# Kernel tuning notes

Measured on AMD Instinct MI355X. Metric: run time of the kernel, lower is better.

The kernel has to match this reference:

```python
import jax, jax.numpy as jnp
import numpy as np

N_COMPANY = 16384
N_SECTOR = 64
PER_SECTOR = N_COMPANY // N_SECTOR  # 256, companies grouped contiguously by sector
WIN = 32
D_IN = 16
H_GRU = 64
H_INTRA = 64
H_INTER = 64
D_OUT = 4
E_INNER = 524288  # avg degree 32 within sectors


def setup_inputs() -> dict:
    key = jax.random.key(0)
    ks = jax.random.split(key, 20)
    s = 0.05

    daily_data_batch = jax.random.normal(ks[0], (WIN, N_COMPANY, D_IN), jnp.float32)

    rng = np.random.default_rng(0)
    dst = rng.integers(0, N_COMPANY, E_INNER)
    src = (dst // PER_SECTOR) * PER_SECTOR + rng.integers(0, PER_SECTOR, E_INNER)  # same-sector neighbors
    inner_edge = jnp.asarray(np.stack([src, dst]), jnp.int32)

    a, b = np.meshgrid(np.arange(N_SECTOR), np.arange(N_SECTOR), indexing="ij")
    oe = np.stack([a.ravel(), b.ravel()])
    oe = oe[:, oe[0] != oe[1]]  # fully-connected sector graph w/o self loops (GAT adds them)
    outer_edge = jnp.asarray(oe, jnp.int32)

    sector_ids = jnp.asarray(np.arange(N_COMPANY) // PER_SECTOR, jnp.int32)

    inp = {
        "daily_data_batch": daily_data_batch,
        "inner_edge": inner_edge,
        "outer_edge": outer_edge,
        "sector_ids": sector_ids,
        # BatchNorm1d(input_dim*window_size)
        "bn_gamma": jnp.ones((D_IN * WIN,), jnp.float32),
        "bn_beta": jnp.zeros((D_IN * WIN,), jnp.float32),
        # Graph GRU (per-node learnable initial hidden state)
        "gru_Wih": s * jax.random.normal(ks[1], (D_IN, 3 * H_GRU), jnp.float32),
        "gru_Whh": s * jax.random.normal(ks[2], (H_GRU, 3 * H_GRU), jnp.float32),
        "gru_bih": jnp.zeros((3 * H_GRU,), jnp.float32),
        "gru_bhh": jnp.zeros((3 * H_GRU,), jnp.float32),
        "gru_h0": s * jax.random.normal(ks[3], (N_COMPANY, H_GRU), jnp.float32),
        # intra-sector GATConv
        "gat1_W": s * jax.random.normal(ks[4], (H_GRU, H_INTRA), jnp.float32),
        "gat1_asrc": s * jax.random.normal(ks[5], (H_INTRA,), jnp.float32),
        "gat1_adst": s * jax.random.normal(ks[6], (H_INTRA,), jnp.float32),
        "gat1_b": jnp.zeros((H_INTRA,), jnp.float32),
        # inter-sector GATConv
        "gat2_W": s * jax.random.normal(ks[7], (H_INTRA, H_INTER), jnp.float32),
        "gat2_asrc": s * jax.random.normal(ks[8], (H_INTER,), jnp.float32),
        "gat2_adst": s * jax.random.normal(ks[9], (H_INTER,), jnp.float32),
        "gat2_b": jnp.zeros((H_INTER,), jnp.float32),
        # fusion / logit heads
        "fusion_W": s * jax.random.normal(ks[10], (H_GRU + H_INTRA + H_INTER, H_GRU), jnp.float32),
        "fusion_b": jnp.zeros((H_GRU,), jnp.float32),
        "logit_W": s * jax.random.normal(ks[11], (H_GRU, D_OUT), jnp.float32),
        "logit_b": jnp.zeros((D_OUT,), jnp.float32),
    }
    return inp


def _gat(x, edge, W, a_src, a_dst, b):
    """PyG-style single-head GATConv with default add_self_loops=True."""
    N = x.shape[0]
    h = x @ W  # [N, F]
    loops = jnp.arange(N, dtype=edge.dtype)
    src = jnp.concatenate([edge[0], loops])
    dst = jnp.concatenate([edge[1], loops])
    e = jax.nn.leaky_relu(h[src] @ a_src + h[dst] @ a_dst, 0.2)  # [E]
    # segment softmax over incoming edges per dst node
    m = jax.ops.segment_max(e, dst, num_segments=N)
    ex = jnp.exp(e - m[dst])
    denom = jax.ops.segment_sum(ex, dst, num_segments=N)
    alpha = ex / (denom[dst] + 1e-16)
    out = jax.ops.segment_sum(h[src] * alpha[:, None], dst, num_segments=N)
    return out + b


def _forward(daily_data_batch, inner_edge, outer_edge, sector_ids,
             bn_gamma, bn_beta,
             gru_Wih, gru_Whh, gru_bih, gru_bhh, gru_h0,
             gat1_W, gat1_asrc, gat1_adst, gat1_b,
             gat2_W, gat2_asrc, gat2_adst, gat2_b,
             fusion_W, fusion_b, logit_W, logit_b):
    W, N, D = daily_data_batch.shape
    # BatchNorm1d over companies (train-mode batch stats, eps=1e-5)
    xb = jnp.transpose(daily_data_batch, (1, 0, 2)).reshape(N, W * D)
    mu = xb.mean(axis=0)
    var = xb.var(axis=0)
    xb = (xb - mu) * jax.lax.rsqrt(var + 1e-5) * bn_gamma + bn_beta
    x = jnp.transpose(xb.reshape(N, W, D), (1, 0, 2))  # [W, N, D]

    # GRU over the window, per-node hidden state
    def step(h, xt):
        gi = xt @ gru_Wih + gru_bih
        gh = h @ gru_Whh + gru_bhh
        ir, iz, inn = jnp.split(gi, 3, axis=-1)
        hr, hz, hn = jnp.split(gh, 3, axis=-1)
        r = jax.nn.sigmoid(ir + hr)
        z = jax.nn.sigmoid(iz + hz)
        n = jnp.tanh(inn + r * hn)
        return (1.0 - z) * n + z * h, None

    seq_emb, _ = jax.lax.scan(step, gru_h0, x)  # [N, H_GRU]

    intra_emb = _gat(seq_emb, inner_edge, gat1_W, gat1_asrc, gat1_adst, gat1_b)  # [N, H_INTRA]

    # sector_separater + per-sector max pooling == segment_max
    sec_pool = jax.ops.segment_max(intra_emb, sector_ids, num_segments=N_SECTOR)  # [S, H_INTRA]
    sec_emb = _gat(sec_pool, outer_edge, gat2_W, gat2_asrc, gat2_adst, gat2_b)  # [S, H_INTER]
    sec_broad = sec_emb[sector_ids]  # repeat_interleave back to companies

    fusion_vec = jnp.concatenate([seq_emb, sec_broad, intra_emb], axis=-1)
    fusion_vec = jax.nn.relu(fusion_vec @ fusion_W + fusion_b)
    logits = jax.nn.softmax(fusion_vec @ logit_W + logit_b, axis=1)
    logits = jnp.cumsum(logits, axis=1)
    eps = 5e-08
    return jnp.clip(logits, eps, 1.0 - eps)


def reference(daily_data_batch, inner_edge, outer_edge, sector_ids,
              bn_gamma, bn_beta,
              gru_Wih, gru_Whh, gru_bih, gru_bhh, gru_h0,
              gat1_W, gat1_asrc, gat1_adst, gat1_b,
              gat2_W, gat2_asrc, gat2_adst, gat2_b,
              fusion_W, fusion_b, logit_W, logit_b):
    return _forward(daily_data_batch, inner_edge, outer_edge, sector_ids,
                    bn_gamma, bn_beta,
                    gru_Wih, gru_Whh, gru_bih, gru_bhh, gru_h0,
                    gat1_W, gat1_asrc, gat1_adst, gat1_b,
                    gat2_W, gat2_asrc, gat2_adst, gat2_b,
                    fusion_W, fusion_b, logit_W, logit_b)
```

## Files before the change

### kernel.cpp

```cpp
#include <hip/hip_runtime.h>

#define NC 16384
#define WIN 32
#define DI 16
#define EI 524288

typedef unsigned short u16;
typedef unsigned char u8;
typedef unsigned int u32;
typedef __attribute__((ext_vector_type(8))) short bfrag8;
typedef __attribute__((ext_vector_type(4))) float facc4;

__device__ __forceinline__ float bf2f(u16 u) { return __uint_as_float(((u32)u) << 16); }
__device__ __forceinline__ u16 f2bf(float f) {
    u32 u = __float_as_uint(f);
    u += 0x7FFFu + ((u >> 16) & 1u);
    return (u16)(u >> 16);
}
__device__ __forceinline__ float frcp(float x) { return __builtin_amdgcn_rcpf(x); }
__device__ __forceinline__ float ex2(float x) {
#if __has_builtin(__builtin_amdgcn_exp2f)
    return __builtin_amdgcn_exp2f(x);
#else
    return __expf(x * 0.69314718055994531f);
#endif
}
__device__ __forceinline__ u32 pk2bf(float a, float b) {
    u32 r;
    asm("v_cvt_pk_bf16_f32 %0, %1, %2" : "=v"(r) : "v"(a), "v"(b));
    return r;
}
__device__ __forceinline__ float lrelu(float x) { return x >= 0.0f ? x : 0.2f * x; }
__device__ __forceinline__ float loadf(const void* p, size_t i, bool f32) {
    return f32 ? ((const float*)p)[i] : bf2f(((const u16*)p)[i]);
}
__device__ __forceinline__ bool is_f32(const void* gamma) {
    return ((const u32*)gamma)[0] == 0x3F800000u;
}

#define O_WIMG  1024
#define O_BIMG  10240
#define O_BIH   16384
#define O_BHH   16576
#define O_G1W   16768
#define O_G1AS  20864
#define O_G1AD  20928
#define O_G1B   20992
#define O_G2W   21056
#define O_G2AS  25152
#define O_G2AD  25216
#define O_G2B   25280
#define O_FB    25344
#define O_LW    25408
#define O_LB    25664
#define O_FW16  25668
#define O_BNACC 31812
#define O_SEQ   40960
#define O_H1    1089536
#define O_INTRA 1613824
#define O_SPOOL 2138112
#define O_AS    2170880
#define O_AD    2187264
#define O_M     2203648

__global__ __launch_bounds__(256) void k_convert(const void* __restrict__ gamma,
                                                 const void* __restrict__ wih,
                                                 const void* __restrict__ whh,
                                                 const void* __restrict__ bih,
                                                 const void* __restrict__ bhh,
                                                 const void* __restrict__ g1w,
                                                 const void* __restrict__ g1as,
                                                 const void* __restrict__ g1ad,
                                                 const void* __restrict__ g1b,
                                                 const void* __restrict__ g2w,
                                                 const void* __restrict__ g2as,
                                                 const void* __restrict__ g2ad,
                                                 const void* __restrict__ g2b,
                                                 const void* __restrict__ fw,
                                                 const void* __restrict__ fb,
                                                 const void* __restrict__ lw,
                                                 const void* __restrict__ lb,
                                                 float* __restrict__ ws,
                                                 uint4* __restrict__ M16) {
    int gt = blockIdx.x * 256 + threadIdx.x;
    const int GS = 64 * 256;
    bool f32 = is_f32(gamma);
    const float KR = -1.4426950408889634f;
    const float KN = -2.8853900817779268f;
    u16* fw16 = (u16*)(ws + O_FW16);
    for (int i = gt; i < 12288; i += GS)
        fw16[i] = f32 ? f2bf(((const float*)fw)[i]) : ((const u16*)fw)[i];
    for (int i = gt; i < 4096; i += GS) {
        ws[O_G1W + i] = loadf(g1w, i, f32);
        ws[O_G2W + i] = loadf(g2w, i, f32);
    }
    if (gt < 64) {
        ws[O_G1AS + gt] = loadf(g1as, gt, f32);
        ws[O_G1AD + gt] = loadf(g1ad, gt, f32);
        ws[O_G1B + gt] = loadf(g1b, gt, f32);
        ws[O_G2AS + gt] = loadf(g2as, gt, f32);
        ws[O_G2AD + gt] = loadf(g2ad, gt, f32);
        ws[O_G2B + gt] = loadf(g2b, gt, f32);
        ws[O_FB + gt] = loadf(fb, gt, f32);
    }
    if (gt < 256) ws[O_LW + gt] = loadf(lw, gt, f32);
    if (gt < 4) ws[O_LB + gt] = loadf(lb, gt, f32);
    for (int i = gt; i < 1024; i += GS) ws[O_BNACC + i] = 0.f;
    const uint4 z4 = {0u, 0u, 0u, 0u};
    for (int i = gt; i < 262144; i += GS) M16[i] = z4;

    for (int i = gt; i < 9216; i += GS) {
        int trow = i / 36;
        int idx = i % 36;
        int w_ = trow >> 6, lane_ = trow & 63, li_ = lane_ & 15, q_ = lane_ >> 4;
        u16 lo, hi;
        if (idx < 24) {
            int g = idx >> 3, kc = (idx >> 2) & 1, j2 = idx & 3;
            float sc = (g < 2) ? KR : KN;
            int col = g * 64 + w_ * 16 + li_;
            int k = kc * 32 + q_ * 8 + j2 * 2;
            lo = f2bf(sc * loadf(whh, (size_t)k * 192 + col, f32));
            hi = f2bf(sc * loadf(whh, (size_t)(k + 1) * 192 + col, f32));
        } else {
            int idx2 = idx - 24;
            int g = idx2 >> 2, j2 = idx2 & 3;
            float sc = (g < 2) ? KR : KN;
            int col = g * 64 + w_ * 16 + li_;
            int k = q_ * 8 + j2 * 2;
            lo = (k < 16) ? f2bf(sc * loadf(wih, (size_t)k * 192 + col, f32)) : (u16)0;
            hi = (k + 1 < 16) ? f2bf(sc * loadf(wih, (size_t)(k + 1) * 192 + col, f32)) : (u16)0;
        }
        ((u32*)(ws + O_WIMG))[i] = (u32)lo | ((u32)hi << 16);
    }
    for (int i = gt; i < 1024; i += GS) {
        int trow = i >> 2, e = i & 3;
        int w_ = trow >> 6, lane_ = trow & 63, li_ = lane_ & 15;
        int c = w_ * 16 + li_;
        float v;
        if (e == 0) v = KR * (loadf(bih, c, f32) + loadf(bhh, c, f32));
        else if (e == 1) v = KR * (loadf(bih, 64 + c, f32) + loadf(bhh, 64 + c, f32));
        else if (e == 2) v = KN * loadf(bih, 128 + c, f32);
        else v = KN * loadf(bhh, 128 + c, f32);
        ws[O_BIMG + i] = v;
    }
}

__global__ __launch_bounds__(256) void k_prep(const void* __restrict__ daily,
                                              const void* __restrict__ gamma,
                                              float* __restrict__ bnacc,
                                              const int* __restrict__ edges,
                                              u32* __restrict__ M32) {
    __shared__ float rS[256 * 17];
    __shared__ float rQ[256 * 17];
    int bid = blockIdx.x;
    int tid = threadIdx.x;
    if (bid >= 128) {
        int g = (bid - 128) * 256 + tid;
        int4 s4 = ((const int4*)edges)[g];
        int4 d4 = ((const int4*)(edges + EI))[g];
        int ss[4] = {s4.x, s4.y, s4.z, s4.w};
        int dd[4] = {d4.x, d4.y, d4.z, d4.w};
#pragma unroll
        for (int i = 0; i < 4; i++) {
            int sl = ss[i] & 255;
            atomicAdd(&M32[dd[i] * 64 + (sl >> 2)], 1u << ((sl & 3) * 8));
        }
        return;
    }
    int w = bid >> 2, ch = bid & 3;
    bool f32 = is_f32(gamma);
    float s[16], q[16];
#pragma unroll
    for (int i = 0; i < 16; i++) { s[i] = 0.f; q[i] = 0.f; }
    for (int it = 0; it < 16; it++) {
        int c = ch * 4096 + it * 256 + tid;
        size_t base = ((size_t)w * NC + c) * DI;
        float v[16];
        if (f32) {
            const float4* p = (const float4*)((const float*)daily + base);
            float4 a = p[0], b = p[1], cc = p[2], d = p[3];
            v[0] = a.x; v[1] = a.y; v[2] = a.z; v[3] = a.w;
            v[4] = b.x; v[5] = b.y; v[6] = b.z; v[7] = b.w;
            v[8] = cc.x; v[9] = cc.y; v[10] = cc.z; v[11] = cc.w;
            v[12] = d.x; v[13] = d.y; v[14] = d.z; v[15] = d.w;
        } else {
            const uint4* p = (const uint4*)((const u16*)daily + base);
            uint4 a = p[0], b = p[1];
            u32 us[8] = {a.x, a.y, a.z, a.w, b.x, b.y, b.z, b.w};
#pragma unroll
            for (int i = 0; i < 8; i++) {
                v[2 * i] = __uint_as_float(us[i] << 16);
                v[2 * i + 1] = __uint_as_float(us[i] & 0xFFFF0000u);
            }
        }
#pragma unroll
        for (int i = 0; i < 16; i++) { s[i] += v[i]; q[i] += v[i] * v[i]; }
    }
#pragma unroll
    for (int i = 0; i < 16; i++) { rS[tid * 17 + i] = s[i]; rQ[tid * 17 + i] = q[i]; }
    __syncthreads();
    int f = tid & 15, g = tid >> 4;
    float ss = 0.f, qq = 0.f;
    for (int t = g * 16; t < g * 16 + 16; t++) { ss += rS[t * 17 + f]; qq += rQ[t * 17 + f]; }
    atomicAdd(&bnacc[w * 16 + f], ss);
    atomicAdd(&bnacc[512 + w * 16 + f], qq);
}

__global__ __launch_bounds__(256) void k_gru(const void* __restrict__ daily,
                                             const void* __restrict__ gamma,
                                             const void* __restrict__ beta,
                                             const void* __restrict__ h0_g,
                                             const float* __restrict__ ws,
                                             float* __restrict__ seq_out,
                                             u16* __restrict__ h1_out,
                                             float* __restrict__ asg,
                                             float* __restrict__ adg) {
    __shared__ __attribute__((aligned(16))) u16 sHd[2][16 * 72];
    __shared__ __attribute__((aligned(16))) u16 sXall[512 * 24];
    __shared__ float sSc[512], sSh[512];
    __shared__ float sRed[2][4][16];
    int tid = threadIdx.x;
    int w = tid >> 6, lane = tid & 63;
    int li = lane & 15, q = lane >> 4;
    int n0 = blockIdx.x * 16;
    int colw = w * 16 + li;
    bool f32 = is_f32(gamma);

    for (int f = tid; f < 512; f += 256) {
        float mu = ws[O_BNACC + f] * (1.0f / NC);
        float var = ws[O_BNACC + 512 + f] * (1.0f / NC) - mu * mu;
        float sc = loadf(gamma, f, f32) * rsqrtf(var + 1e-5f);
        sSc[f] = sc;
        sSh[f] = loadf(beta, f, f32) - mu * sc;
    }
    __syncthreads();

    for (int R = tid; R < 512; R += 256) {
        int t = R >> 4, m = R & 15;
        size_t base = ((size_t)t * NC + n0 + m) * DI;
        float xv[16];
        if (f32) {
            const float4* p = (const float4*)((const float*)daily + base);
            float4 a = p[0], b = p[1], c = p[2], d = p[3];
            xv[0] = a.x; xv[1] = a.y; xv[2] = a.z; xv[3] = a.w;
            xv[4] = b.x; xv[5] = b.y; xv[6] = b.z; xv[7] = b.w;
            xv[8] = c.x; xv[9] = c.y; xv[10] = c.z; xv[11] = c.w;
            xv[12] = d.x; xv[13] = d.y; xv[14] = d.z; xv[15] = d.w;
        } else {
            const uint4* p = (const uint4*)((const u16*)daily + base);
            uint4 a = p[0], b = p[1];
            u32 us[8] = {a.x, a.y, a.z, a.w, b.x, b.y, b.z, b.w};
#pragma unroll
            for (int i = 0; i < 8; i++) {
                xv[2 * i] = __uint_as_float(us[i] << 16);
                xv[2 * i + 1] = __uint_as_float(us[i] & 0xFFFF0000u);
            }
        }
        u32 pxu[8];
#pragma unroll
        for (int i = 0; i < 16; i += 2)
            pxu[i >> 1] = pk2bf(xv[i] * sSc[t * 16 + i] + sSh[t * 16 + i],
                                xv[i + 1] * sSc[t * 16 + i + 1] + sSh[t * 16 + i + 1]);
        *(uint4*)&sXall[R * 24] = *(const uint4*)&pxu[0];
        *(uint4*)&sXall[R * 24 + 8] = *(const uint4*)&pxu[4];
    }

    bfrag8 bh[3][2];
    bfrag8 bx[3];
    {
        const bfrag8* wf = (const bfrag8*)((const char*)(ws + O_WIMG) + (size_t)tid * 144);
        int c_ = 0;
#pragma unroll
        for (int g = 0; g < 3; g++)
#pragma unroll
            for (int kc = 0; kc < 2; kc++) bh[g][kc] = wf[c_++];
#pragma unroll
        for (int g = 0; g < 3; g++) bx[g] = wf[c_++];
    }
    float bR, bZ, bNX, bNH;
    {
        float4 b0 = ((const float4*)(ws + O_BIMG))[tid];
        bR = b0.x; bZ = b0.y; bNX = b0.z; bNH = b0.w;
    }

    float hC[4];
#pragma unroll
    for (int r = 0; r < 4; r++)
        hC[r] = loadf(h0_g, (size_t)(n0 + q * 4 + r) * 64 + colw, f32);
    {
        int hr = tid >> 4, hc = (tid & 15) * 4;
        u32 a = pk2bf(loadf(h0_g, (size_t)(n0 + hr) * 64 + hc, f32),
                      loadf(h0_g, (size_t)(n0 + hr) * 64 + hc + 1, f32));
        u32 b = pk2bf(loadf(h0_g, (size_t)(n0 + hr) * 64 + hc + 2, f32),
                      loadf(h0_g, (size_t)(n0 + hr) * 64 + hc + 3, f32));
        uint2 v2; v2.x = a; v2.y = b;
        *(uint2*)&sHd[0][hr * 72 + hc] = v2;
    }
    __syncthreads();

    bfrag8 ax = (bfrag8){0, 0, 0, 0, 0, 0, 0, 0};
    if (q < 2) ax = *(const bfrag8*)&sXall[li * 24 + q * 8];
    for (int t = 0; t < WIN; t++) {
        int p = t & 1;
        bfrag8 ah0 = *(const bfrag8*)&sHd[p][li * 72 + q * 8];
        bfrag8 ah1 = *(const bfrag8*)&sHd[p][li * 72 + 32 + q * 8];
        int tn = (t + 1) & (WIN - 1);
        bfrag8 axn = (bfrag8){0, 0, 0, 0, 0, 0, 0, 0};
        if (q < 2) axn = *(const bfrag8*)&sXall[(tn * 16 + li) * 24 + q * 8];
        facc4 aR = __builtin_amdgcn_mfma_f32_16x16x32_bf16(ax, bx[0], (facc4){bR, bR, bR, bR}, 0, 0, 0);
        facc4 aZ = __builtin_amdgcn_mfma_f32_16x16x32_bf16(ax, bx[1], (facc4){bZ, bZ, bZ, bZ}, 0, 0, 0);
        facc4 aNX = __builtin_amdgcn_mfma_f32_16x16x32_bf16(ax, bx[2], (facc4){bNX, bNX, bNX, bNX}, 0, 0, 0);
        facc4 aNH = __builtin_amdgcn_mfma_f32_16x16x32_bf16(ah0, bh[2][0], (facc4){bNH, bNH, bNH, bNH}, 0, 0, 0);
        aR = __builtin_amdgcn_mfma_f32_16x16x32_bf16(ah0, bh[0][0], aR, 0, 0, 0);
        aZ = __builtin_amdgcn_mfma_f32_16x16x32_bf16(ah0, bh[1][0], aZ, 0, 0, 0);
        aNH = __builtin_amdgcn_mfma_f32_16x16x32_bf16(ah1, bh[2][1], aNH, 0, 0, 0);
        aR = __builtin_amdgcn_mfma_f32_16x16x32_bf16(ah1, bh[0][1], aR, 0, 0, 0);
        aZ = __builtin_amdgcn_mfma_f32_16x16x32_bf16(ah1, bh[1][1], aZ, 0, 0, 0);
#pragma unroll
        for (int r = 0; r < 4; r++) {
            float gr = frcp(1.0f + ex2(aR[r]));
            float gz = frcp(1.0f + ex2(aZ[r]));
            float narg = aNX[r] + gr * aNH[r];
            float gn = 2.0f * frcp(1.0f + ex2(narg)) - 1.0f;
            hC[r] = gn + gz * (hC[r] - gn);
        }
#pragma unroll
        for (int rp = 0; rp < 4; rp += 2) {
            u32 pk = pk2bf(hC[rp], hC[rp + 1]);
            sHd[p ^ 1][(q * 4 + rp) * 72 + colw] = (u16)pk;
            sHd[p ^ 1][(q * 4 + rp + 1) * 72 + colw] = (u16)(pk >> 16);
        }
        __syncthreads();
        ax = axn;
    }

#pragma unroll
    for (int r = 0; r < 4; r++)
        seq_out[(size_t)(n0 + q * 4 + r) * 64 + colw] = hC[r];

    bfrag8 a0 = *(const bfrag8*)&sHd[0][li * 72 + q * 8];
    bfrag8 a1 = *(const bfrag8*)&sHd[0][li * 72 + 32 + q * 8];
    const facc4 zf = {0.f, 0.f, 0.f, 0.f};
    bfrag8 bg0, bg1;
#pragma unroll
    for (int j = 0; j < 8; j++) {
        bg0[j] = (short)f2bf(ws[O_G1W + (q * 8 + j) * 64 + colw]);
        bg1[j] = (short)f2bf(ws[O_G1W + (32 + q * 8 + j) * 64 + colw]);
    }
    facc4 acc = __builtin_amdgcn_mfma_f32_16x16x32_bf16(a0, bg0, zf, 0, 0, 0);
    acc = __builtin_amdgcn_mfma_f32_16x16x32_bf16(a1, bg1, acc, 0, 0, 0);
    float a1s_j = ws[O_G1AS + colw], a1d_j = ws[O_G1AD + colw];
    float pAs[4], pAd[4];
#pragma unroll
    for (int r = 0; r < 4; r++) {
        h1_out[(size_t)(n0 + q * 4 + r) * 64 + colw] = f2bf(acc[r]);
        pAs[r] = acc[r] * a1s_j;
        pAd[r] = acc[r] * a1d_j;
    }
#pragma unroll
    for (int o = 1; o < 16; o <<= 1)
#pragma unroll
        for (int r = 0; r < 4; r++) {
            pAs[r] += __shfl_xor(pAs[r], o);
            pAd[r] += __shfl_xor(pAd[r], o);
        }
    if (li == 0) {
#pragma unroll
        for (int r = 0; r < 4; r++) {
            sRed[0][w][q * 4 + r] = pAs[r];
            sRed[1][w][q * 4 + r] = pAd[r];
        }
    }
    __syncthreads();
    if (tid < 16) {
        asg[n0 + tid] = sRed[0][0][tid] + sRed[0][1][tid] + sRed[0][2][tid] + sRed[0][3][tid];
        adg[n0 + tid] = sRed[1][0][tid] + sRed[1][1][tid] + sRed[1][2][tid] + sRed[1][3][tid];
    }
}

__global__ __launch_bounds__(256) void k_gat1agg(const u16* __restrict__ h1g,
                                                 const float* __restrict__ ws,
                                                 const u8* __restrict__ M8,
                                                 const float* __restrict__ asg,
                                                 const float* __restrict__ adg,
                                                 u16* __restrict__ intra,
                                                 float* __restrict__ spool8) {
    __shared__ __attribute__((aligned(16))) u16 hT[64 * 264];
    __shared__ __attribute__((aligned(16))) u16 sP[32 * 264];
    __shared__ float sAs[256], sAd[32], sB[64], sRS[32];
    __shared__ float sRSp[8][32];
    __shared__ float wmax[4];
    int tid = threadIdx.x;
    int sector = blockIdx.x >> 3;
    int dstbase = sector * 256 + (blockIdx.x & 7) * 32;
    int sbase = sector * 256;
    {
#pragma unroll
        for (int p = 0; p < 8; p++) {
            int row = p * 32 + (tid >> 3);
            int c0 = (tid & 7) * 8;
            uint4 v = *(const uint4*)(h1g + (size_t)(sbase + row) * 64 + c0);
            u16 e[8];
            *(uint4*)e = v;
#pragma unroll
            for (int i = 0; i < 8; i++) hT[(c0 + i) * 264 + row] = e[i];
        }
    }
    sAs[tid] = asg[sbase + tid];
    if (tid < 32) sAd[tid] = adg[dstbase + tid];
    if (tid < 64) sB[tid] = ws[O_G1B + tid];
    __syncthreads();
    int lane = tid & 63, w = tid >> 6;
    int li = lane & 15, q = lane >> 4;
    {
        float a = sAs[tid];
#pragma unroll
        for (int o = 1; o < 64; o <<= 1) a = fmaxf(a, __shfl_xor(a, o));
        if (lane == 0) wmax[w] = a;
    }
    __syncthreads();
    float maxA = fmaxf(fmaxf(wmax[0], wmax[1]), fmaxf(wmax[2], wmax[3]));

    int prow = tid >> 3, pcg = tid & 7;
    {
        float adr_p = sAd[prow];
        float mrow_p = lrelu(maxA + adr_p);
        float lsum = 0.f;
        const u8* mp = M8 + (size_t)(dstbase + prow) * 256 + pcg * 32;
        uint4 mva = *(const uint4*)mp;
        uint4 mvb = *(const uint4*)(mp + 16);
        u32 wsrc[8] = {mva.x, mva.y, mva.z, mva.w, mvb.x, mvb.y, mvb.z, mvb.w};
#pragma unroll
        for (int i2 = 0; i2 < 16; i2++) {
            int i0 = 2 * i2;
            u32 mb0 = (wsrc[i0 >> 2] >> ((i0 & 3) * 8)) & 255u;
            u32 mb1 = (wsrc[i0 >> 2] >> (((i0 + 1) & 3) * 8)) & 255u;
            int c = pcg * 32 + i0;
            float e0 = lrelu(sAs[c] + adr_p);
            float e1 = lrelu(sAs[c + 1] + adr_p);
            float v0 = (float)mb0 * __expf(e0 - mrow_p);
            float v1 = (float)mb1 * __expf(e1 - mrow_p);
            u16 b0 = f2bf(v0), b1 = f2bf(v1);
            *(u32*)&sP[prow * 264 + pcg * 32 + i0] = (u32)b0 | ((u32)b1 << 16);
            lsum += bf2f(b0) + bf2f(b1);
        }
        sRSp[pcg][prow] = lsum;
    }
    __syncthreads();

    facc4 acc[2];
    acc[0] = (facc4){0.f, 0.f, 0.f, 0.f};
    acc[1] = (facc4){0.f, 0.f, 0.f, 0.f};
#pragma unroll
    for (int kc = 0; kc < 8; kc++) {
        bfrag8 bfh = *(const bfrag8*)&hT[(w * 16 + li) * 264 + kc * 32 + q * 8];
#pragma unroll
        for (int mt = 0; mt < 2; mt++) {
            bfrag8 af = *(const bfrag8*)&sP[(mt * 16 + li) * 264 + kc * 32 + q * 8];
            acc[mt] = __builtin_amdgcn_mfma_f32_16x16x32_bf16(af, bfh, acc[mt], 0, 0, 0);
        }
    }
    if (tid < 32) {
        float s = 0.f;
#pragma unroll
        for (int g = 0; g < 8; g++) s += sRSp[g][tid];
        sRS[tid] = s;
    }
    __syncthreads();

    float vmax = -1e30f;
    int colL = w * 16 + li;
#pragma unroll
    for (int mt = 0; mt < 2; mt++) {
#pragma unroll
        for (int r = 0; r < 4; r++) {
            int row = mt * 16 + q * 4 + r;
            int d = dstbase + row;
            int selfI = (blockIdx.x & 7) * 32 + row;
            float adr = sAd[row];
            float es = lrelu(sAs[selfI] + adr);
            float mrow = lrelu(maxA + adr);
            float exS = __expf(es - mrow);
            float denom = sRS[row] + exS;
            float inv = frcp(denom + 1e-16f);
            float selfh = bf2f(hT[colL * 264 + selfI]);
            float val = (acc[mt][r] + exS * selfh) * inv + sB[colL];
            intra[(size_t)d * 64 + colL] = f2bf(val);
            vmax = fmaxf(vmax, val);
        }
    }
    vmax = fmaxf(vmax, __shfl_xor(vmax, 16));
    vmax = fmaxf(vmax, __shfl_xor(vmax, 32));
    if (q == 0) spool8[(size_t)blockIdx.x * 64 + colL] = vmax;
}

__global__ __launch_bounds__(256) void k_fusion(const float* __restrict__ seq,
                                                const float* __restrict__ spool8,
                                                const u16* __restrict__ intra,
                                                const float* __restrict__ ws,
                                                const void* __restrict__ gamma,
                                                void* __restrict__ out) {
    __shared__ __attribute__((aligned(16))) union {
        struct { u16 sPmax[64 * 72]; float sH2[64 * 68]; } p0;
        struct { u16 sV[64 * 200]; float sFus[64 * 68]; } p1;
    } U;
    __shared__ float sSemb[64], sAs2[64], sAd2[64];
    __shared__ float sFB[64], sLW[256], sLB[4];
    __shared__ float red2[512];
    int tid = threadIdx.x, n0 = blockIdx.x * 64;
    int sid = blockIdx.x >> 2;
    bool f32 = is_f32(gamma);
    int lane = tid & 63, w = tid >> 6;
    int li = lane & 15, q = lane >> 4;
    int colw = w * 16 + li;

    for (int i = tid; i < 4096; i += 256) {
        int n = i >> 6, k = i & 63;
        const float* pp = &spool8[(size_t)(n * 8) * 64 + k];
        float m = pp[0];
#pragma unroll
        for (int p = 1; p < 8; p++) m = fmaxf(m, pp[p * 64]);
        U.p0.sPmax[n * 72 + k] = f2bf(m);
    }
    bfrag8 bw2[2];
#pragma unroll
    for (int kc = 0; kc < 2; kc++)
#pragma unroll
        for (int j = 0; j < 8; j++)
            bw2[kc][j] = (short)f2bf(ws[O_G2W + (kc * 32 + q * 8 + j) * 64 + colw]);
    __syncthreads();
    {
        const facc4 zf = {0.f, 0.f, 0.f, 0.f};
#pragma unroll
        for (int mt = 0; mt < 4; mt++) {
            bfrag8 af0 = *(const bfrag8*)&U.p0.sPmax[(mt * 16 + li) * 72 + q * 8];
            bfrag8 af1 = *(const bfrag8*)&U.p0.sPmax[(mt * 16 + li) * 72 + 32 + q * 8];
            facc4 a2 = __builtin_amdgcn_mfma_f32_16x16x32_bf16(af0, bw2[0], zf, 0, 0, 0);
            a2 = __builtin_amdgcn_mfma_f32_16x16x32_bf16(af1, bw2[1], a2, 0, 0, 0);
#pragma unroll
            for (int r = 0; r < 4; r++)
                U.p0.sH2[(mt * 16 + q * 4 + r) * 68 + colw] = a2[r];
        }
    }
    __syncthreads();
    {
        int n = tid >> 2, jg = tid & 3, j0 = jg * 16;
        float ps = 0.f, pd = 0.f;
#pragma unroll
        for (int i = 0; i < 16; i++) {
            float v = U.p0.sH2[n * 68 + j0 + i];
            ps += v * ws[O_G2AS + j0 + i];
            pd += v * ws[O_G2AD + j0 + i];
        }
        red2[(n * 4 + jg) * 2] = ps;
        red2[(n * 4 + jg) * 2 + 1] = pd;
    }
    __syncthreads();
    if (tid < 64) {
        float s = 0.f, dd = 0.f;
        for (int g = 0; g < 4; g++) { s += red2[(tid * 4 + g) * 2]; dd += red2[(tid * 4 + g) * 2 + 1]; }
        sAs2[tid] = s; sAd2[tid] = dd;
    }
    __syncthreads();
    if (tid < 64) {
        float e = lrelu(sAs2[tid] + sAd2[sid]);
        float m = e;
        for (int o = 32; o; o >>= 1) m = fmaxf(m, __shfl_xor(m, o));
        float ex = __expf(e - m);
        float den = ex;
        for (int o = 32; o; o >>= 1) den += __shfl_xor(den, o);
        float inv = frcp(den + 1e-16f);
        float o_ = 0.f;
        for (int l = 0; l < 64; l++) {
            float a = __shfl(ex, l);
            o_ += a * U.p0.sH2[l * 68 + tid];
        }
        sSemb[tid] = o_ * inv + ws[O_G2B + tid];
    }
    if (tid < 64) sFB[tid] = ws[O_FB + tid];
    sLW[tid] = ws[O_LW + tid];
    if (tid < 4) sLB[tid] = ws[O_LB + tid];
    __syncthreads();

    {
        int c = tid >> 2, p = tid & 3;
        u16 px[16];
        const float* rp = seq + (size_t)(n0 + c) * 64 + p * 16;
#pragma unroll
        for (int i = 0; i < 16; i += 4) {
            float4 v = *(const float4*)&rp[i];
            px[i] = f2bf(v.x); px[i + 1] = f2bf(v.y); px[i + 2] = f2bf(v.z); px[i + 3] = f2bf(v.w);
        }
        *(uint4*)&U.p1.sV[c * 200 + p * 16] = *(const uint4*)&px[0];
        *(uint4*)&U.p1.sV[c * 200 + p * 16 + 8] = *(const uint4*)&px[8];
#pragma unroll
        for (int i = 0; i < 16; i++) px[i] = f2bf(sSemb[p * 16 + i]);
        *(uint4*)&U.p1.sV[c * 200 + 64 + p * 16] = *(const uint4*)&px[0];
        *(uint4*)&U.p1.sV[c * 200 + 64 + p * 16 + 8] = *(const uint4*)&px[8];
        const u16* ip = intra + (size_t)(n0 + c) * 64 + p * 16;
        *(uint4*)&U.p1.sV[c * 200 + 128 + p * 16] = *(const uint4*)ip;
        *(uint4*)&U.p1.sV[c * 200 + 128 + p * 16 + 8] = *(const uint4*)(ip + 8);
    }
    const u16* fw16g = (const u16*)(ws + O_FW16);
    bfrag8 bwf[6];
#pragma unroll
    for (int kc = 0; kc < 6; kc++)
#pragma unroll
        for (int j = 0; j < 8; j++)
            bwf[kc][j] = (short)fw16g[(kc * 32 + q * 8 + j) * 64 + colw];
    __syncthreads();

    facc4 acc[4];
#pragma unroll
    for (int mt = 0; mt < 4; mt++) acc[mt] = (facc4){0.f, 0.f, 0.f, 0.f};
#pragma unroll
    for (int kc = 0; kc < 6; kc++) {
#pragma unroll
        for (int mt = 0; mt < 4; mt++) {
            bfrag8 av = *(const bfrag8*)&U.p1.sV[(mt * 16 + li) * 200 + kc * 32 + q * 8];
            acc[mt] = __builtin_amdgcn_mfma_f32_16x16x32_bf16(av, bwf[kc], acc[mt], 0, 0, 0);
        }
    }
    float fb = sFB[colw];
#pragma unroll
    for (int mt = 0; mt < 4; mt++)
#pragma unroll
        for (int r = 0; r < 4; r++) {
            float v = fmaxf(acc[mt][r] + fb, 0.f);
            U.p1.sFus[(mt * 16 + q * 4 + r) * 68 + colw] = v;
        }
    __syncthreads();

    {
        int cpy = tid >> 2, cls = tid & 3;
        float lv = sLB[cls];
        for (int j = 0; j < 64; j++) lv += U.p1.sFus[cpy * 68 + j] * sLW[j * 4 + cls];
        float m2 = fmaxf(lv, __shfl_xor(lv, 1));
        m2 = fmaxf(m2, __shfl_xor(m2, 2));
        float e = __expf(lv - m2);
        float s2 = e + __shfl_xor(e, 1);
        s2 += __shfl_xor(s2, 2);
        float is = frcp(s2);
        float pref = e;
        float t1 = __shfl_up(pref, 1);
        if (cls >= 1) pref += t1;
        float t2 = __shfl_up(pref, 2);
        if (cls >= 2) pref += t2;
        float ck = pref * is;
        const float lo = 5e-8f, hi = 1.0f - 5e-8f;
        ck = fminf(fmaxf(ck, lo), hi);
        size_t ob = (size_t)(n0 + cpy) * 4 + cls;
        if (f32) ((float*)out)[ob] = ck;
        else ((u16*)out)[ob] = f2bf(ck);
    }
}

extern "C" void kernel_launch(void* const* d_in, const int* in_sizes, int n_in,
                              void* d_out, int out_size, void* d_ws, size_t ws_size,
                              hipStream_t stream) {
    const void* daily = d_in[0];
    const int* inner = (const int*)d_in[1];
    const void* gamma = d_in[4];
    const void* beta = d_in[5];
    const void* wih = d_in[6];
    const void* whh = d_in[7];
    const void* bih = d_in[8];
    const void* bhh = d_in[9];
    const void* h0 = d_in[10];
    const void* g1w = d_in[11];
    const void* g1as = d_in[12];
    const void* g1ad = d_in[13];
    const void* g1b = d_in[14];
    const void* g2w = d_in[15];
    const void* g2as = d_in[16];
    const void* g2ad = d_in[17];
    const void* g2b = d_in[18];
    const void* fw = d_in[19];
    const void* fb = d_in[20];
    const void* lw = d_in[21];
    const void* lb = d_in[22];

    float* ws = (float*)d_ws;
    u16* h1g = (u16*)(ws + O_H1);
    u16* intra = (u16*)(ws + O_INTRA);
    u8* M8 = (u8*)(ws + O_M);

    k_convert<<<64, 256, 0, stream>>>(gamma, wih, whh, bih, bhh, g1w, g1as, g1ad, g1b,
                                      g2w, g2as, g2ad, g2b, fw, fb, lw, lb, ws, (uint4*)M8);
    k_prep<<<640, 256, 0, stream>>>(daily, gamma, ws + O_BNACC, inner, (u32*)M8);
    k_gru<<<1024, 256, 0, stream>>>(daily, gamma, beta, h0, ws, ws + O_SEQ, h1g, ws + O_AS, ws + O_AD);
    k_gat1agg<<<512, 256, 0, stream>>>(h1g, ws, M8, ws + O_AS, ws + O_AD, intra, ws + O_SPOOL);
    k_fusion<<<256, 256, 0, stream>>>(ws + O_SEQ, ws + O_SPOOL, intra, ws, gamma, d_out);
}
```

Before: 217.5 us.

## Merge convert and prep kernels, drop BN atomics, swizzle transposed LDS tile

```diff
diff --git a/kernel.cpp b/kernel.cpp
--- a/kernel.cpp
+++ b/kernel.cpp
@@ -37,6 +37,7 @@
 __device__ __forceinline__ bool is_f32(const void* gamma) {
     return ((const u32*)gamma)[0] == 0x3F800000u;
 }
+__device__ __forceinline__ int hswz(int f, int s) { return s ^ (((f >> 3) & 3) << 3); }
 
 #define O_WIMG  1024
 #define O_BIMG  10240
@@ -63,7 +64,10 @@
 #define O_AD    2187264
 #define O_M     2203648
 
-__global__ __launch_bounds__(256) void k_convert(const void* __restrict__ gamma,
+__global__ __launch_bounds__(256) void k_convert(const void* __restrict__ daily,
+                                                 const int* __restrict__ edges,
+                                                 u32* __restrict__ M32,
+                                                 const void* __restrict__ gamma,
                                                  const void* __restrict__ wih,
                                                  const void* __restrict__ whh,
                                                  const void* __restrict__ bih,
@@ -80,13 +84,32 @@
                                                  const void* __restrict__ fb,
                                                  const void* __restrict__ lw,
                                                  const void* __restrict__ lb,
-                                                 float* __restrict__ ws,
-                                                 uint4* __restrict__ M16) {
-    int gt = blockIdx.x * 256 + threadIdx.x;
-    const int GS = 64 * 256;
+                                                 float* __restrict__ ws) {
+    __shared__ float rS[256 * 17];
+    __shared__ float rQ[256 * 17];
+    __shared__ float sOut[2][16][16];
+    int bid = blockIdx.x;
+    int tid = threadIdx.x;
+    int gt = bid * 256 + tid;
+    const int GS = 640 * 256;
     bool f32 = is_f32(gamma);
     const float KR = -1.4426950408889634f;
     const float KN = -2.8853900817779268f;
+
+    if (bid >= 128) {
+        int g = (bid - 128) * 256 + tid;
+        int4 s4 = ((const int4*)edges)[g];
+        int4 d4 = ((const int4*)(edges + EI))[g];
+        int ss[4] = {s4.x, s4.y, s4.z, s4.w};
+        int dd[4] = {d4.x, d4.y, d4.z, d4.w};
+#pragma unroll
+        for (int i = 0; i < 4; i++) {
+            int sl = ss[i] & 255;
+            atomicAdd(&M32[dd[i] * 64 + (sl >> 2)], 1u << ((sl & 3) * 8));
+        }
+        return;
+    }
+
     u16* fw16 = (u16*)(ws + O_FW16);
     for (int i = gt; i < 12288; i += GS)
         fw16[i] = f32 ? f2bf(((const float*)fw)[i]) : ((const u16*)fw)[i];
@@ -105,9 +128,6 @@
     }
     if (gt < 256) ws[O_LW + gt] = loadf(lw, gt, f32);
     if (gt < 4) ws[O_LB + gt] = loadf(lb, gt, f32);
-    for (int i = gt; i < 1024; i += GS) ws[O_BNACC + i] = 0.f;
-    const uint4 z4 = {0u, 0u, 0u, 0u};
-    for (int i = gt; i < 262144; i += GS) M16[i] = z4;
 
     for (int i = gt; i < 9216; i += GS) {
         int trow = i / 36;
@@ -143,67 +163,53 @@
         else v = KN * loadf(bhh, 128 + c, f32);
         ws[O_BIMG + i] = v;
     }
-}
-
-__global__ __launch_bounds__(256) void k_prep(const void* __restrict__ daily,
-                                              const void* __restrict__ gamma,
-                                              float* __restrict__ bnacc,
-                                              const int* __restrict__ edges,
-                                              u32* __restrict__ M32) {
-    __shared__ float rS[256 * 17];
-    __shared__ float rQ[256 * 17];
-    int bid = blockIdx.x;
-    int tid = threadIdx.x;
-    if (bid >= 128) {
-        int g = (bid - 128) * 256 + tid;
-        int4 s4 = ((const int4*)edges)[g];
-        int4 d4 = ((const int4*)(edges + EI))[g];
-        int ss[4] = {s4.x, s4.y, s4.z, s4.w};
-        int dd[4] = {d4.x, d4.y, d4.z, d4.w};
-#pragma unroll
-        for (int i = 0; i < 4; i++) {
-            int sl = ss[i] & 255;
-            atomicAdd(&M32[dd[i] * 64 + (sl >> 2)], 1u << ((sl & 3) * 8));
-        }
-        return;
-    }
-    int w = bid >> 2, ch = bid & 3;
-    bool f32 = is_f32(gamma);
-    float s[16], q[16];
-#pragma unroll
-    for (int i = 0; i < 16; i++) { s[i] = 0.f; q[i] = 0.f; }
-    for (int it = 0; it < 16; it++) {
-        int c = ch * 4096 + it * 256 + tid;
-        size_t base = ((size_t)w * NC + c) * DI;
-        float v[16];
-        if (f32) {
-            const float4* p = (const float4*)((const float*)daily + base);
-            float4 a = p[0], b = p[1], cc = p[2], d = p[3];
-            v[0] = a.x; v[1] = a.y; v[2] = a.z; v[3] = a.w;
-            v[4] = b.x; v[5] = b.y; v[6] = b.z; v[7] = b.w;
-            v[8] = cc.x; v[9] = cc.y; v[10] = cc.z; v[11] = cc.w;
-            v[12] = d.x; v[13] = d.y; v[14] = d.z; v[15] = d.w;
-        } else {
-            const uint4* p = (const uint4*)((const u16*)daily + base);
-            uint4 a = p[0], b = p[1];
-            u32 us[8] = {a.x, a.y, a.z, a.w, b.x, b.y, b.z, b.w};
-#pragma unroll
-            for (int i = 0; i < 8; i++) {
-                v[2 * i] = __uint_as_float(us[i] << 16);
-                v[2 * i + 1] = __uint_as_float(us[i] & 0xFFFF0000u);
+
+    {
+        int w = bid >> 2, ch = bid & 3;
+        float s[16], q[16];
+#pragma unroll
+        for (int i = 0; i < 16; i++) { s[i] = 0.f; q[i] = 0.f; }
+        for (int it = 0; it < 16; it++) {
+            int c = ch * 4096 + it * 256 + tid;
+            size_t base = ((size_t)w * NC + c) * DI;
+            float v[16];
+            if (f32) {
+                const float4* p = (const float4*)((const float*)daily + base);
+                float4 a = p[0], b = p[1], cc = p[2], d = p[3];
+                v[0] = a.x; v[1] = a.y; v[2] = a.z; v[3] = a.w;
+                v[4] = b.x; v[5] = b.y; v[6] = b.z; v[7] = b.w;
+                v[8] = cc.x; v[9] = cc.y; v[10] = cc.z; v[11] = cc.w;
+                v[12] = d.x; v[13] = d.y; v[14] = d.z; v[15] = d.w;
+            } else {
+                const uint4* p = (const uint4*)((const u16*)daily + base);
+                uint4 a = p[0], b = p[1];
+                u32 us[8] = {a.x, a.y, a.z, a.w, b.x, b.y, b.z, b.w};
+#pragma unroll
+                for (int i = 0; i < 8; i++) {
+                    v[2 * i] = __uint_as_float(us[i] << 16);
+                    v[2 * i + 1] = __uint_as_float(us[i] & 0xFFFF0000u);
+                }
             }
-        }
-#pragma unroll
-        for (int i = 0; i < 16; i++) { s[i] += v[i]; q[i] += v[i] * v[i]; }
-    }
-#pragma unroll
-    for (int i = 0; i < 16; i++) { rS[tid * 17 + i] = s[i]; rQ[tid * 17 + i] = q[i]; }
-    __syncthreads();
-    int f = tid & 15, g = tid >> 4;
-    float ss = 0.f, qq = 0.f;
-    for (int t = g * 16; t < g * 16 + 16; t++) { ss += rS[t * 17 + f]; qq += rQ[t * 17 + f]; }
-    atomicAdd(&bnacc[w * 16 + f], ss);
-    atomicAdd(&bnacc[512 + w * 16 + f], qq);
+#pragma unroll
+            for (int i = 0; i < 16; i++) { s[i] += v[i]; q[i] += v[i] * v[i]; }
+        }
+#pragma unroll
+        for (int i = 0; i < 16; i++) { rS[tid * 17 + i] = s[i]; rQ[tid * 17 + i] = q[i]; }
+        __syncthreads();
+        int f = tid & 15, g = tid >> 4;
+        float ss = 0.f, qq = 0.f;
+        for (int t = g * 16; t < g * 16 + 16; t++) { ss += rS[t * 17 + f]; qq += rQ[t * 17 + f]; }
+        sOut[0][g][f] = ss;
+        sOut[1][g][f] = qq;
+        __syncthreads();
+        if (tid < 16) {
+            float S = 0.f, Q = 0.f;
+#pragma unroll
+            for (int g2 = 0; g2 < 16; g2++) { S += sOut[0][g2][tid]; Q += sOut[1][g2][tid]; }
+            ws[O_BNACC + ch * 512 + w * 16 + tid] = S;
+            ws[O_BNACC + 2048 + ch * 512 + w * 16 + tid] = Q;
+        }
+    }
 }
 
 __global__ __launch_bounds__(256) void k_gru(const void* __restrict__ daily,
@@ -227,8 +233,10 @@
     bool f32 = is_f32(gamma);
 
     for (int f = tid; f < 512; f += 256) {
-        float mu = ws[O_BNACC + f] * (1.0f / NC);
-        float var = ws[O_BNACC + 512 + f] * (1.0f / NC) - mu * mu;
+        float S = ws[O_BNACC + f] + ws[O_BNACC + 512 + f] + ws[O_BNACC + 1024 + f] + ws[O_BNACC + 1536 + f];
+        float Q = ws[O_BNACC + 2048 + f] + ws[O_BNACC + 2560 + f] + ws[O_BNACC + 3072 + f] + ws[O_BNACC + 3584 + f];
+        float mu = S * (1.0f / NC);
+        float var = Q * (1.0f / NC) - mu * mu;
         float sc = loadf(gamma, f, f32) * rsqrtf(var + 1e-5f);
         sSc[f] = sc;
         sSh[f] = loadf(beta, f, f32) - mu * sc;
@@ -403,7 +411,10 @@
             u16 e[8];
             *(uint4*)e = v;
 #pragma unroll
-            for (int i = 0; i < 8; i++) hT[(c0 + i) * 264 + row] = e[i];
+            for (int i = 0; i < 8; i++) {
+                int f = c0 + i;
+                hT[f * 264 + hswz(f, row)] = e[i];
+            }
         }
     }
     sAs[tid] = asg[sbase + tid];
@@ -453,7 +464,8 @@
     acc[1] = (facc4){0.f, 0.f, 0.f, 0.f};
 #pragma unroll
     for (int kc = 0; kc < 8; kc++) {
-        bfrag8 bfh = *(const bfrag8*)&hT[(w * 16 + li) * 264 + kc * 32 + q * 8];
+        int fB = w * 16 + li;
+        bfrag8 bfh = *(const bfrag8*)&hT[fB * 264 + hswz(fB, kc * 32 + q * 8)];
 #pragma unroll
         for (int mt = 0; mt < 2; mt++) {
             bfrag8 af = *(const bfrag8*)&sP[(mt * 16 + li) * 264 + kc * 32 + q * 8];
@@ -483,7 +495,7 @@
             float exS = __expf(es - mrow);
             float denom = sRS[row] + exS;
             float inv = frcp(denom + 1e-16f);
-            float selfh = bf2f(hT[colL * 264 + selfI]);
+            float selfh = bf2f(hT[colL * 264 + hswz(colL, selfI)]);
             float val = (acc[mt][r] + exS * selfh) * inv + sB[colL];
             intra[(size_t)d * 64 + colL] = f2bf(val);
             vmax = fmaxf(vmax, val);
@@ -685,9 +697,10 @@
     u16* intra = (u16*)(ws + O_INTRA);
     u8* M8 = (u8*)(ws + O_M);
 
-    k_convert<<<64, 256, 0, stream>>>(gamma, wih, whh, bih, bhh, g1w, g1as, g1ad, g1b,
-                                      g2w, g2as, g2ad, g2b, fw, fb, lw, lb, ws, (uint4*)M8);
-    k_prep<<<640, 256, 0, stream>>>(daily, gamma, ws + O_BNACC, inner, (u32*)M8);
+    hipMemsetAsync(M8, 0, (size_t)NC * 256, stream);
+    k_convert<<<640, 256, 0, stream>>>(daily, inner, (u32*)M8, gamma, wih, whh, bih, bhh,
+                                       g1w, g1as, g1ad, g1b, g2w, g2as, g2ad, g2b,
+                                       fw, fb, lw, lb, ws);
     k_gru<<<1024, 256, 0, stream>>>(daily, gamma, beta, h0, ws, ws + O_SEQ, h1g, ws + O_AS, ws + O_AD);
     k_gat1agg<<<512, 256, 0, stream>>>(h1g, ws, M8, ws + O_AS, ws + O_AD, intra, ws + O_SPOOL);
     k_fusion<<<256, 256, 0, stream>>>(ws + O_SEQ, ws + O_SPOOL, intra, ws, gamma, d_out);
```

New measurement: 208.1 us. -4.3%, faster.
